# Optimization experiments

Measured on AMD Instinct MI355X. Metric: run time of the kernel, lower is better.

## Reference

```python
import jax, jax.numpy as jnp
import numpy as np

T, N, E, F0, F1 = 8, 100000, 3200000, 16, 16


def setup_inputs() -> dict:
    key = jax.random.key(0)
    ks = jax.random.split(key, 18)
    inp = {}
    inp["X"] = jax.random.normal(ks[0], (T, N, F0), jnp.float32)
    inp["edge_row"] = jax.random.randint(ks[1], (T, E), 0, N, jnp.int32)
    inp["edge_col"] = jax.random.randint(ks[2], (T, E), 0, N, jnp.int32)
    inp["edge_val"] = jax.random.uniform(ks[3], (T, E), jnp.float32)
    inp["p"] = jax.random.normal(ks[4], (F0,), jnp.float32)
    names = ["W_Z", "U_Z", "B_Z", "W_R", "U_R", "B_R", "W_H", "U_H", "B_H", "W_init"]
    for i, n in enumerate(names):
        inp[n] = jax.random.normal(ks[5 + i], (F0, F1 if n.startswith("B") or n == "W_init" else F0), jnp.float32)
    inp["lin_w"] = jax.random.normal(ks[15], (F1,), jnp.float32)
    inp["lin_b"] = jax.random.normal(ks[16], (1,), jnp.float32)
    return inp


def reference(X, edge_row, edge_col, edge_val, p, W_Z, U_Z, B_Z, W_R, U_R, B_R, W_H, U_H, B_H, W_init, lin_w, lin_b):
    def step(W, xs):
        X_t, row, col, val = xs  # X_t: [N, F0]; row/col/val: [E]
        # summarize: topk-weighted row selection, k = F1
        y = (X_t @ p) / jnp.linalg.norm(p)              # [N]
        yk, idx = jax.lax.top_k(y, F1)                  # sorted desc, matches torch.topk
        Xs = (X_t[idx] * yk[:, None]).T                 # [F0, F1]
        # GRU on the weight matrix W: [F0, F1]
        Zg = jax.nn.sigmoid(W_Z @ Xs + U_Z @ W + B_Z)
        Rg = jax.nn.sigmoid(W_R @ Xs + U_R @ W + B_R)
        Ht = jnp.tanh(W_H @ Xs + U_H @ (Rg * W) + B_H)
        W_new = (1.0 - Zg) * W + Zg * Ht
        # sparse GCONV: (A @ X_t) @ W_new via gather + segment_sum
        AH = jax.ops.segment_sum(val[:, None] * X_t[col], row, num_segments=N)  # [N, F0]
        H_new = AH @ W_new                              # [N, F1]
        return W_new, H_new

    _, Y = jax.lax.scan(step, W_init, (X, edge_row, edge_col, edge_val))  # Y: [T, N, F1]
    return Y @ lin_w + lin_b[0]                          # [T, N]
```

## Files before the change

kernel.cpp:

```cpp
#include <hip/hip_runtime.h>
#include <stdint.h>

#define T_STEPS 8
#define N_NODES 100000
#define E_EDGES 3200000
#define NB1 250
#define CHUNK 400
#define NB3 391
#define NCAND_T 4000
#define NSLICE 8
#define ESLICE (E_EDGES / NSLICE)
#define RNG_BITS 15
#define RNG (1 << RNG_BITS)
#define NRNG 4
#define SC_BLKS (T_STEPS * NRNG * NSLICE)

__device__ __forceinline__ uint16_t f2bf(float x) {
    uint32_t b = __float_as_uint(x);
    b += 0x7FFFu + ((b >> 16) & 1u);
    return (uint16_t)(b >> 16);
}
__device__ __forceinline__ float bf2f(uint16_t u) {
    return __uint_as_float(((uint32_t)u) << 16);
}

__device__ __forceinline__ unsigned long long make_key(float v, int idx) {
    uint32_t u = __float_as_uint(v);
    u = (u & 0x80000000u) ? ~u : (u | 0x80000000u);
    return (((unsigned long long)u) << 32) | (unsigned long long)(~(uint32_t)idx);
}
__device__ __forceinline__ float key_val(unsigned long long k) {
    uint32_t u = (uint32_t)(k >> 32);
    u = (u & 0x80000000u) ? (u & 0x7FFFFFFFu) : ~u;
    return __uint_as_float(u);
}
__device__ __forceinline__ int key_idx(unsigned long long k) {
    return (int)(~(uint32_t)(k & 0xFFFFFFFFu));
}

__device__ __forceinline__ unsigned long long shfl_xor_u64(unsigned long long x, int mask) {
    uint32_t lo = (uint32_t)x, hi = (uint32_t)(x >> 32);
    lo = __shfl_xor((unsigned int)lo, mask);
    hi = __shfl_xor((unsigned int)hi, mask);
    return (((unsigned long long)hi) << 32) | lo;
}

__device__ __forceinline__ void wave_argmax(unsigned long long& m, int& mp) {
    #pragma unroll
    for (int off = 32; off; off >>= 1) {
        unsigned long long o = shfl_xor_u64(m, off);
        int op = __shfl_xor(mp, off);
        if (o > m) { m = o; mp = op; }
    }
}

__device__ __forceinline__ float dot16(const float4* __restrict__ xr, const float* w) {
    float4 a = xr[0], b = xr[1], c = xr[2], d = xr[3];
    return a.x*w[0] + a.y*w[1] + a.z*w[2] + a.w*w[3]
         + b.x*w[4] + b.y*w[5] + b.z*w[6] + b.w*w[7]
         + c.x*w[8] + c.y*w[9] + c.z*w[10] + c.w*w[11]
         + d.x*w[12] + d.y*w[13] + d.z*w[14] + d.w*w[15];
}

__global__ __launch_bounds__(256) void k_y_topk_all(const float* __restrict__ X,
                                                    const float* __restrict__ p,
                                                    unsigned long long* __restrict__ cand) {
    __shared__ unsigned long long keys[CHUNK];
    __shared__ unsigned long long wm[4];
    __shared__ int wp[4];
    int tid = threadIdx.x;
    int t = blockIdx.x / NB1;
    int b = blockIdx.x % NB1;
    const float* Xt = X + (size_t)t * N_NODES * 16;
    float pv[16];
    #pragma unroll
    for (int i = 0; i < 16; i++) pv[i] = p[i];
    float pn = 0.f;
    #pragma unroll
    for (int i = 0; i < 16; i++) pn += pv[i] * pv[i];
    float inv = 1.0f / sqrtf(pn);
    int base = b * CHUNK;
    for (int i = tid; i < CHUNK; i += 256) {
        int n = base + i;
        float y = dot16((const float4*)(Xt + (size_t)n * 16), pv) * inv;
        keys[i] = make_key(y, n);
    }
    __syncthreads();
    for (int k = 0; k < 16; k++) {
        unsigned long long m = 0ULL; int mp = -1;
        for (int i = tid; i < CHUNK; i += 256) {
            unsigned long long v = keys[i];
            if (v > m) { m = v; mp = i; }
        }
        wave_argmax(m, mp);
        if ((tid & 63) == 0) { wm[tid >> 6] = m; wp[tid >> 6] = mp; }
        __syncthreads();
        if (tid == 0) {
            unsigned long long best = wm[0]; int bp = wp[0];
            #pragma unroll
            for (int w2 = 1; w2 < 4; w2++) if (wm[w2] > best) { best = wm[w2]; bp = wp[w2]; }
            cand[(size_t)t * NCAND_T + b * 16 + k] = best;
            keys[bp] = 0ULL;
        }
        __syncthreads();
    }
}

__global__ __launch_bounds__(512) void k_merge_gru(
    const unsigned long long* __restrict__ cand,
    const float* __restrict__ X,
    const float* __restrict__ Winit,
    const float* __restrict__ W_Z, const float* __restrict__ U_Z, const float* __restrict__ B_Z,
    const float* __restrict__ W_R, const float* __restrict__ U_R, const float* __restrict__ B_R,
    const float* __restrict__ W_H, const float* __restrict__ U_H, const float* __restrict__ B_H,
    const float* __restrict__ lin_w,
    float* __restrict__ weff_g) {
    __shared__ float mWZ[256], mUZ[256], mBZ[256], mWR[256], mUR[256], mBR[256];
    __shared__ float mWH[256], mUH[256], mBH[256], mLW[16];
    __shared__ int   sidx[8][16];
    __shared__ float sval[8][16];
    __shared__ float Xs_all[8][16][16];
    __shared__ float Wcur[16][16];
    __shared__ float RgW[16][16];
    int tid = threadIdx.x;
    if (tid < 256) {
        mWZ[tid] = W_Z[tid]; mUZ[tid] = U_Z[tid]; mBZ[tid] = B_Z[tid];
        mWR[tid] = W_R[tid]; mUR[tid] = U_R[tid]; mBR[tid] = B_R[tid];
        mWH[tid] = W_H[tid]; mUH[tid] = U_H[tid]; mBH[tid] = B_H[tid];
        Wcur[tid >> 4][tid & 15] = Winit[tid];
        if (tid < 16) mLW[tid] = lin_w[tid];
    }
    {
        int w = tid >> 6, lane = tid & 63;
        const unsigned long long* ct = cand + (size_t)w * NCAND_T;
        int cb = lane * 4;
        unsigned long long h0 = 0, h1 = 0, h2 = 0, h3 = 0;
        int p0 = 0, p1 = 0, p2 = 0, p3 = 0;
        if (cb + 0 < NB1) h0 = ct[(cb + 0) * 16];
        if (cb + 1 < NB1) h1 = ct[(cb + 1) * 16];
        if (cb + 2 < NB1) h2 = ct[(cb + 2) * 16];
        if (cb + 3 < NB1) h3 = ct[(cb + 3) * 16];
        for (int k = 0; k < 16; k++) {
            unsigned long long m = h0; int pay = (lane << 2) | 0;
            if (h1 > m) { m = h1; pay = (lane << 2) | 1; }
            if (h2 > m) { m = h2; pay = (lane << 2) | 2; }
            if (h3 > m) { m = h3; pay = (lane << 2) | 3; }
            wave_argmax(m, pay);
            if (lane == 0) { sidx[w][k] = key_idx(m); sval[w][k] = key_val(m); }
            if ((pay >> 2) == lane) {
                switch (pay & 3) {
                case 0: p0++; h0 = (p0 < 16) ? ct[(cb + 0) * 16 + p0] : 0ULL; break;
                case 1: p1++; h1 = (p1 < 16) ? ct[(cb + 1) * 16 + p1] : 0ULL; break;
                case 2: p2++; h2 = (p2 < 16) ? ct[(cb + 2) * 16 + p2] : 0ULL; break;
                default: p3++; h3 = (p3 < 16) ? ct[(cb + 3) * 16 + p3] : 0ULL; break;
                }
            }
        }
    }
    __syncthreads();
    for (int e = tid; e < 8 * 256; e += 512) {
        int tt = e >> 8, kk = (e >> 4) & 15, ff = e & 15;
        Xs_all[tt][ff][kk] = X[(size_t)tt * N_NODES * 16 + (size_t)sidx[tt][kk] * 16 + ff]
                           * sval[tt][kk];
    }
    __syncthreads();
    int i = (tid & 255) >> 4, j = tid & 15;
    for (int t = 0; t < T_STEPS; t++) {
        float Zg = 0.f, wn = 0.f;
        if (tid < 256) {
            float az = 0.f, ar = 0.f, uz = 0.f, ur = 0.f;
            #pragma unroll
            for (int m = 0; m < 16; m++) {
                az += mWZ[i * 16 + m] * Xs_all[t][m][j];
                ar += mWR[i * 16 + m] * Xs_all[t][m][j];
                uz += mUZ[i * 16 + m] * Wcur[m][j];
                ur += mUR[i * 16 + m] * Wcur[m][j];
            }
            Zg = 1.0f / (1.0f + expf(-(az + uz + mBZ[i * 16 + j])));
            float Rg = 1.0f / (1.0f + expf(-(ar + ur + mBR[i * 16 + j])));
            RgW[i][j] = Rg * Wcur[i][j];
        }
        __syncthreads();
        if (tid < 256) {
            float ah = 0.f, uh = 0.f;
            #pragma unroll
            for (int m = 0; m < 16; m++) {
                ah += mWH[i * 16 + m] * Xs_all[t][m][j];
                uh += mUH[i * 16 + m] * RgW[m][j];
            }
            float Ht = tanhf(ah + uh + mBH[i * 16 + j]);
            wn = (1.0f - Zg) * Wcur[i][j] + Zg * Ht;
        }
        __syncthreads();
        if (tid < 256) Wcur[i][j] = wn;
        __syncthreads();
        if (tid < 16) {
            float acc = 0.f;
            #pragma unroll
            for (int jj = 0; jj < 16; jj++) acc += Wcur[tid][jj] * mLW[jj];
            weff_g[t * 16 + tid] = acc;
        }
        __syncthreads();
    }
}

__global__ __launch_bounds__(256) void k_s_all(const float* __restrict__ X,
                                               const float* __restrict__ weff,
                                               float* __restrict__ s) {
    int t = blockIdx.x / NB3;
    int b = blockIdx.x % NB3;
    __shared__ float w[16];
    if (threadIdx.x < 16) w[threadIdx.x] = weff[t * 16 + threadIdx.x];
    __syncthreads();
    int n = b * 256 + threadIdx.x;
    if (n < N_NODES) {
        float v = dot16((const float4*)(X + ((size_t)t * N_NODES + n) * 16), w);
        s[(size_t)t * N_NODES + n] = v;
    }
}

extern "C" __global__ __launch_bounds__(1024) void k_scatter_fused(
    const int* __restrict__ erow, const int* __restrict__ ecol,
    const float* __restrict__ evalv, const float* __restrict__ s,
    uint16_t* __restrict__ rep) {
    extern __shared__ float acc[];
    const int bid = blockIdx.x;
    const int t = bid & 7;
    const int m = bid >> 3;
    const int slice = m >> 2;
    const int r = m & 3;
    const int base = r << RNG_BITS;
    const int tid = threadIdx.x;
    {
        float4* a4 = (float4*)acc;
        #pragma unroll
        for (int q = 0; q < RNG / 4 / 1024; q++)
            a4[tid + q * 1024] = make_float4(0.f, 0.f, 0.f, 0.f);
    }
    __syncthreads();
    const float* __restrict__ st = s + (size_t)t * N_NODES;
    const size_t eb = (size_t)t * E_EDGES + (size_t)slice * ESLICE;
    const int4* __restrict__ r4 = (const int4*)(erow + eb);
    const int4* __restrict__ c4 = (const int4*)(ecol + eb);
    const float4* __restrict__ v4 = (const float4*)(evalv + eb);
    const int n4 = ESLICE / 4;
    const int half = n4 / 2;

    for (int i = tid; i < half; i += 1024) {
        int4   Ra = r4[i];          int4   Rb = r4[i + half];
        int4   Ca = c4[i];          int4   Cb = c4[i + half];
        float4 Va = v4[i];          float4 Vb = v4[i + half];
        __builtin_amdgcn_sched_barrier(0);
        int la0 = Ra.x - base, la1 = Ra.y - base, la2 = Ra.z - base, la3 = Ra.w - base;
        bool a0 = (unsigned)la0 < (unsigned)RNG, a1 = (unsigned)la1 < (unsigned)RNG,
             a2 = (unsigned)la2 < (unsigned)RNG, a3 = (unsigned)la3 < (unsigned)RNG;
        int lb0 = Rb.x - base, lb1 = Rb.y - base, lb2 = Rb.z - base, lb3 = Rb.w - base;
        bool b0 = (unsigned)lb0 < (unsigned)RNG, b1 = (unsigned)lb1 < (unsigned)RNG,
             b2 = (unsigned)lb2 < (unsigned)RNG, b3 = (unsigned)lb3 < (unsigned)RNG;
        float ga0 = st[a0 ? Ca.x : 0], ga1 = st[a1 ? Ca.y : 0],
              ga2 = st[a2 ? Ca.z : 0], ga3 = st[a3 ? Ca.w : 0];
        float gb0 = st[b0 ? Cb.x : 0], gb1 = st[b1 ? Cb.y : 0],
              gb2 = st[b2 ? Cb.z : 0], gb3 = st[b3 ? Cb.w : 0];
        __builtin_amdgcn_sched_barrier(0);
        if (a0) atomicAdd(&acc[la0], Va.x * ga0);
        if (a1) atomicAdd(&acc[la1], Va.y * ga1);
        if (a2) atomicAdd(&acc[la2], Va.z * ga2);
        if (a3) atomicAdd(&acc[la3], Va.w * ga3);
        if (b0) atomicAdd(&acc[lb0], Vb.x * gb0);
        if (b1) atomicAdd(&acc[lb1], Vb.y * gb1);
        if (b2) atomicAdd(&acc[lb2], Vb.z * gb2);
        if (b3) atomicAdd(&acc[lb3], Vb.w * gb3);
    }
    __syncthreads();
    const int seg = t * 32 + m;
    ushort4* rp4 = (ushort4*)(rep + (size_t)seg * RNG);
    float4* a4 = (float4*)acc;
    #pragma unroll
    for (int q = 0; q < RNG / 4 / 1024; q++) {
        float4 a = a4[tid + q * 1024];
        ushort4 u;
        u.x = f2bf(a.x); u.y = f2bf(a.y); u.z = f2bf(a.z); u.w = f2bf(a.w);
        rp4[tid + q * 1024] = u;
    }
}

__global__ __launch_bounds__(256) void k_reduce_full(const uint16_t* __restrict__ rep,
                                                     const float* __restrict__ lin_b,
                                                     float* __restrict__ out) {
    int t = blockIdx.x / NB3;
    int b = blockIdx.x % NB3;
    int n = b * 256 + threadIdx.x;
    if (n >= N_NODES) return;
    int r = n >> RNG_BITS;
    int local = n & (RNG - 1);
    float acc = lin_b[0];
    #pragma unroll
    for (int sl = 0; sl < NSLICE; sl++) {
        int seg = t * 32 + sl * 4 + r;
        acc += bf2f(rep[(size_t)seg * RNG + local]);
    }
    out[(size_t)t * N_NODES + n] = acc;
}

extern "C" void kernel_launch(void* const* d_in, const int* in_sizes, int n_in,
                              void* d_out, int out_size, void* d_ws, size_t ws_size,
                              hipStream_t stream) {
    const float* X     = (const float*)d_in[0];
    const int*   erow  = (const int*)d_in[1];
    const int*   ecol  = (const int*)d_in[2];
    const float* evalv = (const float*)d_in[3];
    const float* p     = (const float*)d_in[4];
    const float* W_Z   = (const float*)d_in[5];
    const float* U_Z   = (const float*)d_in[6];
    const float* B_Z   = (const float*)d_in[7];
    const float* W_R   = (const float*)d_in[8];
    const float* U_R   = (const float*)d_in[9];
    const float* B_R   = (const float*)d_in[10];
    const float* W_H   = (const float*)d_in[11];
    const float* U_H   = (const float*)d_in[12];
    const float* B_H   = (const float*)d_in[13];
    const float* Winit = (const float*)d_in[14];
    const float* lin_w = (const float*)d_in[15];
    const float* lin_b = (const float*)d_in[16];
    float* out = (float*)d_out;

    size_t dynLDS = (size_t)RNG * sizeof(float);
    (void)hipFuncSetAttribute((const void*)k_scatter_fused,
                              hipFuncAttributeMaxDynamicSharedMemorySize,
                              (int)dynLDS);

    char* ws = (char*)d_ws;
    float* s    = (float*)ws;
    float* weff = (float*)(ws + 3200000);
    unsigned long long* cand = (unsigned long long*)(ws + 3201024);
    uint16_t* rep = (uint16_t*)(ws + 3457024);

    k_y_topk_all<<<T_STEPS * NB1, 256, 0, stream>>>(X, p, cand);
    k_merge_gru<<<1, 512, 0, stream>>>(cand, X, Winit,
                                       W_Z, U_Z, B_Z, W_R, U_R, B_R, W_H, U_H, B_H,
                                       lin_w, weff);
    k_s_all<<<T_STEPS * NB3, 256, 0, stream>>>(X, weff, s);
    k_scatter_fused<<<SC_BLKS, 1024, dynLDS, stream>>>(erow, ecol, evalv, s, rep);
    k_reduce_full<<<T_STEPS * NB3, 256, 0, stream>>>(rep, lin_b, out);
}
```

Before: 260.1 us.

## Interleave row ownership mod 4 and software-pipeline edge loads in scatter

```diff
diff --git a/kernel.cpp b/kernel.cpp
--- a/kernel.cpp
+++ b/kernel.cpp
@@ -10,9 +10,8 @@
 #define NCAND_T 4000
 #define NSLICE 8
 #define ESLICE (E_EDGES / NSLICE)
-#define RNG_BITS 15
-#define RNG (1 << RNG_BITS)
 #define NRNG 4
+#define ACCN 25000
 #define SC_BLKS (T_STEPS * NRNG * NSLICE)
 
 __device__ __forceinline__ uint16_t f2bf(float x) {
@@ -229,14 +228,8 @@
     const int m = bid >> 3;
     const int slice = m >> 2;
     const int r = m & 3;
-    const int base = r << RNG_BITS;
     const int tid = threadIdx.x;
-    {
-        float4* a4 = (float4*)acc;
-        #pragma unroll
-        for (int q = 0; q < RNG / 4 / 1024; q++)
-            a4[tid + q * 1024] = make_float4(0.f, 0.f, 0.f, 0.f);
-    }
+    for (int i = tid; i < ACCN; i += 1024) acc[i] = 0.f;
     __syncthreads();
     const float* __restrict__ st = s + (size_t)t * N_NODES;
     const size_t eb = (size_t)t * E_EDGES + (size_t)slice * ESLICE;
@@ -244,44 +237,55 @@
     const int4* __restrict__ c4 = (const int4*)(ecol + eb);
     const float4* __restrict__ v4 = (const float4*)(evalv + eb);
     const int n4 = ESLICE / 4;
-    const int half = n4 / 2;
-
-    for (int i = tid; i < half; i += 1024) {
-        int4   Ra = r4[i];          int4   Rb = r4[i + half];
-        int4   Ca = c4[i];          int4   Cb = c4[i + half];
-        float4 Va = v4[i];          float4 Vb = v4[i + half];
+    const int S = (n4 + 1023) >> 10;
+
+    int j0 = tid;
+    int j1 = tid + 1024;
+    int jc0 = j0 < n4 ? j0 : n4 - 1;
+    int jc1 = j1 < n4 ? j1 : n4 - 1;
+    int4   R1 = r4[jc0]; int4 C1 = c4[jc0]; float4 V1 = v4[jc0];
+    int4   R2 = r4[jc1]; int4 C2 = c4[jc1]; float4 V2 = v4[jc1];
+    bool va0 = (j0 < n4) && ((R1.x & 3) == r);
+    bool va1 = (j0 < n4) && ((R1.y & 3) == r);
+    bool va2 = (j0 < n4) && ((R1.z & 3) == r);
+    bool va3 = (j0 < n4) && ((R1.w & 3) == r);
+    int  la0 = R1.x >> 2, la1 = R1.y >> 2, la2 = R1.z >> 2, la3 = R1.w >> 2;
+    float ga0 = va0 ? st[C1.x] : 0.f;
+    float ga1 = va1 ? st[C1.y] : 0.f;
+    float ga2 = va2 ? st[C1.z] : 0.f;
+    float ga3 = va3 ? st[C1.w] : 0.f;
+
+    #pragma unroll 1
+    for (int k = 0; k < S; ++k) {
+        int jn = tid + ((k + 2) << 10);
+        int jcn = jn < n4 ? jn : n4 - 1;
+        int4   Rn = r4[jcn]; int4 Cn = c4[jcn]; float4 Vn = v4[jcn];
         __builtin_amdgcn_sched_barrier(0);
-        int la0 = Ra.x - base, la1 = Ra.y - base, la2 = Ra.z - base, la3 = Ra.w - base;
-        bool a0 = (unsigned)la0 < (unsigned)RNG, a1 = (unsigned)la1 < (unsigned)RNG,
-             a2 = (unsigned)la2 < (unsigned)RNG, a3 = (unsigned)la3 < (unsigned)RNG;
-        int lb0 = Rb.x - base, lb1 = Rb.y - base, lb2 = Rb.z - base, lb3 = Rb.w - base;
-        bool b0 = (unsigned)lb0 < (unsigned)RNG, b1 = (unsigned)lb1 < (unsigned)RNG,
-             b2 = (unsigned)lb2 < (unsigned)RNG, b3 = (unsigned)lb3 < (unsigned)RNG;
-        float ga0 = st[a0 ? Ca.x : 0], ga1 = st[a1 ? Ca.y : 0],
-              ga2 = st[a2 ? Ca.z : 0], ga3 = st[a3 ? Ca.w : 0];
-        float gb0 = st[b0 ? Cb.x : 0], gb1 = st[b1 ? Cb.y : 0],
-              gb2 = st[b2 ? Cb.z : 0], gb3 = st[b3 ? Cb.w : 0];
+        bool vok = (tid + ((k + 1) << 10)) < n4;
+        bool vb0 = vok && ((R2.x & 3) == r);
+        bool vb1 = vok && ((R2.y & 3) == r);
+        bool vb2 = vok && ((R2.z & 3) == r);
+        bool vb3 = vok && ((R2.w & 3) == r);
+        int  lb0 = R2.x >> 2, lb1 = R2.y >> 2, lb2 = R2.z >> 2, lb3 = R2.w >> 2;
+        float gb0 = vb0 ? st[C2.x] : 0.f;
+        float gb1 = vb1 ? st[C2.y] : 0.f;
+        float gb2 = vb2 ? st[C2.z] : 0.f;
+        float gb3 = vb3 ? st[C2.w] : 0.f;
         __builtin_amdgcn_sched_barrier(0);
-        if (a0) atomicAdd(&acc[la0], Va.x * ga0);
-        if (a1) atomicAdd(&acc[la1], Va.y * ga1);
-        if (a2) atomicAdd(&acc[la2], Va.z * ga2);
-        if (a3) atomicAdd(&acc[la3], Va.w * ga3);
-        if (b0) atomicAdd(&acc[lb0], Vb.x * gb0);
-        if (b1) atomicAdd(&acc[lb1], Vb.y * gb1);
-        if (b2) atomicAdd(&acc[lb2], Vb.z * gb2);
-        if (b3) atomicAdd(&acc[lb3], Vb.w * gb3);
+        if (va0) atomicAdd(&acc[la0], V1.x * ga0);
+        if (va1) atomicAdd(&acc[la1], V1.y * ga1);
+        if (va2) atomicAdd(&acc[la2], V1.z * ga2);
+        if (va3) atomicAdd(&acc[la3], V1.w * ga3);
+        va0 = vb0; va1 = vb1; va2 = vb2; va3 = vb3;
+        la0 = lb0; la1 = lb1; la2 = lb2; la3 = lb3;
+        ga0 = gb0; ga1 = gb1; ga2 = gb2; ga3 = gb3;
+        V1 = V2;
+        R2 = Rn; C2 = Cn; V2 = Vn;
     }
     __syncthreads();
     const int seg = t * 32 + m;
-    ushort4* rp4 = (ushort4*)(rep + (size_t)seg * RNG);
-    float4* a4 = (float4*)acc;
-    #pragma unroll
-    for (int q = 0; q < RNG / 4 / 1024; q++) {
-        float4 a = a4[tid + q * 1024];
-        ushort4 u;
-        u.x = f2bf(a.x); u.y = f2bf(a.y); u.z = f2bf(a.z); u.w = f2bf(a.w);
-        rp4[tid + q * 1024] = u;
-    }
+    uint16_t* rp = rep + (size_t)seg * ACCN;
+    for (int i = tid; i < ACCN; i += 1024) rp[i] = f2bf(acc[i]);
 }
 
 __global__ __launch_bounds__(256) void k_reduce_full(const uint16_t* __restrict__ rep,
@@ -291,13 +295,13 @@
     int b = blockIdx.x % NB3;
     int n = b * 256 + threadIdx.x;
     if (n >= N_NODES) return;
-    int r = n >> RNG_BITS;
-    int local = n & (RNG - 1);
+    int r = n & 3;
+    int local = n >> 2;
     float acc = lin_b[0];
     #pragma unroll
     for (int sl = 0; sl < NSLICE; sl++) {
         int seg = t * 32 + sl * 4 + r;
-        acc += bf2f(rep[(size_t)seg * RNG + local]);
+        acc += bf2f(rep[(size_t)seg * ACCN + local]);
     }
     out[(size_t)t * N_NODES + n] = acc;
 }
@@ -324,7 +328,7 @@
     const float* lin_b = (const float*)d_in[16];
     float* out = (float*)d_out;
 
-    size_t dynLDS = (size_t)RNG * sizeof(float);
+    size_t dynLDS = (size_t)ACCN * sizeof(float);
     (void)hipFuncSetAttribute((const void*)k_scatter_fused,
                               hipFuncAttributeMaxDynamicSharedMemorySize,
                               (int)dynLDS);
```

Measured after the change: 273.6 us. 1.05x slower.
